# Kernel tuning notes

Measured on AMD Instinct MI355X. Metric: run time of the kernel, lower is better.

## Reference

```python
import jax, jax.numpy as jnp
import numpy as np

B = 128      # puzzles per batch
CELLS = 81
N = B * CELLS
H = 96       # hidden_dim
E_SZ = 16    # embed_size
T = 16       # num_steps


def _sudoku_edges():
    r = np.arange(CELLS) // 9
    c = np.arange(CELLS) % 9
    b = (r // 3) * 3 + (c // 3)
    src, dst = [], []
    for u in range(CELLS):
        for v in range(CELLS):
            if u != v and (r[u] == r[v] or c[u] == c[v] or b[u] == b[v]):
                src.append(u)
                dst.append(v)
    return np.asarray(src, np.int32), np.asarray(dst, np.int32)


def setup_inputs() -> dict:
    key = jax.random.key(0)
    ks = jax.random.split(key, 24)
    s, d = _sudoku_edges()
    off = (np.arange(B, dtype=np.int32) * CELLS)[:, None]
    src = jnp.asarray((s[None, :] + off).reshape(-1))
    dst = jnp.asarray((d[None, :] + off).reshape(-1))
    row = jnp.asarray(np.tile(np.arange(CELLS, dtype=np.int32) // 9, B))
    col = jnp.asarray(np.tile(np.arange(CELLS, dtype=np.int32) % 9, B))
    q = jax.random.randint(ks[0], (N,), 0, 10, dtype=jnp.int32)
    labels = jax.random.randint(ks[1], (N,), 1, 10, dtype=jnp.int32)

    def lin(k, o, i):
        return (jax.random.normal(k, (o, i), jnp.float32) / np.sqrt(i)).astype(jnp.float32)

    d_emb = jax.random.normal(ks[2], (10, E_SZ), jnp.float32)
    r_emb = jax.random.normal(ks[3], (9, E_SZ), jnp.float32)
    c_emb = jax.random.normal(ks[4], (9, E_SZ), jnp.float32)
    in_W0 = lin(ks[5], H, 3 * E_SZ)
    in_W = jnp.stack([lin(ks[6 + i], H, H) for i in range(3)])   # [3,H,H]
    in_b = jnp.zeros((4, H), jnp.float32)
    msg_W0 = lin(ks[9], H, 2 * H)
    msg_W = jnp.stack([lin(ks[10 + i], H, H) for i in range(3)])
    msg_b = jnp.zeros((4, H), jnp.float32)
    # LSTMCell (no bias): input = cat(x, m) of size 2H, hidden H; gate order i,f,g,o
    W_ih = lin(ks[13], 4 * H, 2 * H)
    W_hh = lin(ks[14], 4 * H, H)
    out_W = lin(ks[15], 10, H)
    out_b = jnp.zeros((10,), jnp.float32)
    return dict(q=q, row=row, col=col, labels=labels, src=src, dst=dst,
                d_emb=d_emb, r_emb=r_emb, c_emb=c_emb,
                in_W0=in_W0, in_W=in_W, in_b=in_b,
                msg_W0=msg_W0, msg_W=msg_W, msg_b=msg_b,
                W_ih=W_ih, W_hh=W_hh, out_W=out_W, out_b=out_b)


def _mlp4(x, W0, W, b):
    # Linear,ReLU,Linear,ReLU,Linear,ReLU,Linear
    x = jax.nn.relu(x @ W0.T + b[0])
    x = jax.nn.relu(x @ W[0].T + b[1])
    x = jax.nn.relu(x @ W[1].T + b[2])
    return x @ W[2].T + b[3]


def reference(q, row, col, labels, src, dst, d_emb, r_emb, c_emb,
              in_W0, in_W, in_b, msg_W0, msg_W, msg_b,
              W_ih, W_hh, out_W, out_b):
    x = _mlp4(jnp.concatenate([d_emb[q], r_emb[row], c_emb[col]], -1),
              in_W0, in_W, in_b)                       # [N,H]
    h0 = x
    rh0 = jnp.zeros_like(x)
    rc0 = jnp.zeros_like(x)

    def step(carry, _):
        h, rh, rc = carry
        # per-edge message: MLP(cat(h_src, h_dst)), sum-aggregated into dst
        me = _mlp4(jnp.concatenate([h[src], h[dst]], -1), msg_W0, msg_W, msg_b)
        m = jax.ops.segment_sum(me, dst, num_segments=N)  # [N,H]
        gates = jnp.concatenate([x, m], -1) @ W_ih.T + rh @ W_hh.T
        i, f, g, o = jnp.split(gates, 4, axis=-1)
        nc = jax.nn.sigmoid(f) * rc + jax.nn.sigmoid(i) * jnp.tanh(g)
        nh = jax.nn.sigmoid(o) * jnp.tanh(nc)
        return (nh, nh, nc), nh

    _, hs = jax.lax.scan(step, (h0, rh0, rc0), None, length=T)  # [T,N,H]
    logits = hs @ out_W.T + out_b                               # [T,N,10]
    preds = jnp.argmax(logits, -1)                              # [T,N]
    lf = logits.reshape(-1, 10)
    lab = jnp.tile(labels, T)
    logp = jax.nn.log_softmax(lf, -1)
    loss = -jnp.mean(jnp.take_along_axis(logp, lab[:, None].astype(jnp.int32), 1))
    return preds, loss, lf
```

## Files before the change

### kernel.cpp

```cpp
#include <hip/hip_runtime.h>

#define NN 10368
#define EE 207360
#define TT 16

#define O_W0AT    0
#define O_W0BT    9216
#define O_WHHT    18432
#define O_WIHXT   55296
#define O_WCOMBT  92160
#define O_GB      129024
#define O_LOSS    129408
#define O_WIN0T   129424
#define O_WINT    134032
#define O_H       161680
#define O_C       (O_H  + NN*96)
#define O_A       (O_C  + NN*96)
#define O_BV      (O_A  + NN*96)
#define O_S2      (O_BV + NN*96)
#define O_X       (O_S2 + NN*96)
#define O_WFRAG   (O_X  + NN*96)
#define O_GX      (O_WFRAG + 27648)
#define O_WL2     O_X
#define O_WAB2    (O_X + 110592)
#define SF_WIN0   O_S2
#define SF_WIN    (O_S2 + 9216)
#define SF_WX     (O_S2 + 50688)

using bf16x8 = __attribute__((ext_vector_type(8))) short;
using s16x4  = __attribute__((ext_vector_type(4))) short;
using f32x4  = __attribute__((ext_vector_type(4))) float;

__device__ __forceinline__ float sigm(float x){ return 1.f/(1.f + expf(-x)); }

__device__ __forceinline__ unsigned rne_bf16(float f){
  unsigned u = __float_as_uint(f);
  u += 0x7fffu + ((u >> 16) & 1u);
  return u >> 16;
}
__device__ __forceinline__ void split3(float x, short& h, short& m, short& l){
  unsigned uh = rne_bf16(x); h = (short)uh;
  float fh = __uint_as_float(uh << 16);
  float r1 = x - fh;
  unsigned um = rne_bf16(r1); m = (short)um;
  float fm = __uint_as_float(um << 16);
  float r2 = r1 - fm;
  l = (short)rne_bf16(r2);
}

__device__ __forceinline__ f32x4 mfma6(bf16x8 aH, bf16x8 aM, bf16x8 aL,
                                       bf16x8 WH, bf16x8 WM, bf16x8 WL, f32x4 acc){
  acc = __builtin_amdgcn_mfma_f32_16x16x32_bf16(aH, WH, acc, 0,0,0);
  acc = __builtin_amdgcn_mfma_f32_16x16x32_bf16(aH, WM, acc, 0,0,0);
  acc = __builtin_amdgcn_mfma_f32_16x16x32_bf16(aM, WH, acc, 0,0,0);
  acc = __builtin_amdgcn_mfma_f32_16x16x32_bf16(aH, WL, acc, 0,0,0);
  acc = __builtin_amdgcn_mfma_f32_16x16x32_bf16(aL, WH, acc, 0,0,0);
  acc = __builtin_amdgcn_mfma_f32_16x16x32_bf16(aM, WM, acc, 0,0,0);
  return acc;
}

__device__ __forceinline__ f32x4 mfma6s(bf16x8 WH, bf16x8 WM, bf16x8 WL,
                                        bf16x8 aH, bf16x8 aM, bf16x8 aL, f32x4 acc){
  acc = __builtin_amdgcn_mfma_f32_16x16x32_bf16(WH, aH, acc, 0,0,0);
  acc = __builtin_amdgcn_mfma_f32_16x16x32_bf16(WM, aH, acc, 0,0,0);
  acc = __builtin_amdgcn_mfma_f32_16x16x32_bf16(WH, aM, acc, 0,0,0);
  acc = __builtin_amdgcn_mfma_f32_16x16x32_bf16(WL, aH, acc, 0,0,0);
  acc = __builtin_amdgcn_mfma_f32_16x16x32_bf16(WH, aL, acc, 0,0,0);
  acc = __builtin_amdgcn_mfma_f32_16x16x32_bf16(WM, aM, acc, 0,0,0);
  return acc;
}

__global__ void k_convert(float* ws, const float* msgW0, const float* Whh, const float* Wih,
                          const float* inW0, const float* inW)
{
  int i = blockIdx.x*256 + threadIdx.x;
  if (i < 9216){ int k=i/96, j=i%96; ws[O_W0AT+i] = msgW0[j*192+k];    return; } i -= 9216;
  if (i < 9216){ int k=i/96, j=i%96; ws[O_W0BT+i] = msgW0[j*192+96+k]; return; } i -= 9216;
  if (i < 36864){ int k=i/384, j=i%384; ws[O_WHHT+i]  = Whh[j*96+k];   return; } i -= 36864;
  if (i < 36864){ int k=i/384, j=i%384; ws[O_WIHXT+i] = Wih[j*192+k];  return; } i -= 36864;
  if (i < 4608){ int k=i/96, j=i%96; ws[O_WIN0T+i] = inW0[j*48+k];     return; } i -= 4608;
  if (i < 27648){ int l=i/9216, r=i%9216; int k=r/96, j=r%96;
                  ws[O_WINT+i] = inW[l*9216 + j*96 + k];               return; } i -= 27648;
  if (i == 0){ ws[O_LOSS] = 0.f; }
}

__global__ void k_wfrag(float* ws, const float* msgW)
{
  int idx = blockIdx.x*256 + threadIdx.x;
  if (idx >= 2*3*18*64) return;
  int lane = idx & 63;
  int tile = (idx >> 6) % 18;
  int lev  = (idx >> 6) / 18 % 3;
  int layer= (idx >> 6) / 54;
  int nt = tile/3, kt = tile%3;
  int nout = (lane & 15) + 16*nt;
  int q = lane >> 4;
  unsigned short* wf = (unsigned short*)(ws + O_WFRAG);
  unsigned short* dstp = wf + (size_t)(((layer*3+lev)*18 + tile)*64 + lane)*8;
  const float* W = msgW + layer*9216;
  for (int j=0;j<8;j++){
    float wv = W[nout*96 + 32*kt + 8*q + j];
    short h,m,l; split3(wv, h, m, l);
    dstp[j] = (unsigned short)(lev==0 ? h : (lev==1 ? m : l));
  }
}

__global__ void k_wcomb(float* ws, const float* Wih, const float* msgW, const float* msgb)
{
  int t = blockIdx.x*256 + threadIdx.x;
  if (t >= 36864) return;
  int j = t % 384, qq = t / 384;
  float a0=0.f,a1=0.f,a2=0.f,a3=0.f;
  for (int r=0;r<96;r+=4){
    a0 = fmaf(Wih[j*192+96+r  ], msgW[2*9216+(r  )*96+qq], a0);
    a1 = fmaf(Wih[j*192+96+r+1], msgW[2*9216+(r+1)*96+qq], a1);
    a2 = fmaf(Wih[j*192+96+r+2], msgW[2*9216+(r+2)*96+qq], a2);
    a3 = fmaf(Wih[j*192+96+r+3], msgW[2*9216+(r+3)*96+qq], a3);
  }
  ws[O_WCOMBT + qq*384 + j] = (a0+a1)+(a2+a3);
  if (qq == 0){
    float g=0.f;
    for (int r=0;r<96;r++) g = fmaf(Wih[j*192+96+r], msgb[288+r], g);
    ws[O_GB + j] = 20.f * g;
  }
}

__global__ void k_wl(float* ws)
{
  int idx = blockIdx.x*256 + threadIdx.x;
  if (idx >= 24*6*64) return;
  int L  = idx & 63;
  int ks = (idx >> 6) % 6;
  int nt = (idx >> 6) / 6;
  int col = (L & 15) + 16*nt;
  int q = L >> 4;
  unsigned short* wf = (unsigned short*)(ws + O_WL2);
  for (int j=0;j<8;j++){
    int k = 32*(ks%3) + 8*q + j;
    float wv = (ks < 3) ? ws[O_WCOMBT + k*384 + col] : ws[O_WHHT + k*384 + col];
    short h,m,l; split3(wv, h, m, l);
    wf[(size_t)(((0*24+nt)*6 + ks)*64 + L)*8 + j] = (unsigned short)h;
    wf[(size_t)(((1*24+nt)*6 + ks)*64 + L)*8 + j] = (unsigned short)m;
    wf[(size_t)(((2*24+nt)*6 + ks)*64 + L)*8 + j] = (unsigned short)l;
  }
}

__global__ void k_wab(float* ws)
{
  int idx = blockIdx.x*256 + threadIdx.x;
  if (idx >= 12*3*64) return;
  int L  = idx & 63;
  int ks = (idx >> 6) % 3;
  int nt = (idx >> 6) / 3;
  int col = (L & 15) + 16*nt;
  int q = L >> 4;
  unsigned short* wf = (unsigned short*)(ws + O_WAB2);
  for (int j=0;j<8;j++){
    int k = 32*ks + 8*q + j;
    float wv = (col < 96) ? ws[O_W0AT + k*96 + col] : ws[O_W0BT + k*96 + (col-96)];
    short h,m,l; split3(wv, h, m, l);
    wf[(size_t)(((0*12+nt)*3 + ks)*64 + L)*8 + j] = (unsigned short)h;
    wf[(size_t)(((1*12+nt)*3 + ks)*64 + L)*8 + j] = (unsigned short)m;
    wf[(size_t)(((2*12+nt)*3 + ks)*64 + L)*8 + j] = (unsigned short)l;
  }
}

__global__ void k_wfin(float* ws)
{
  int idx = blockIdx.x*256 + threadIdx.x;
  if (idx >= 138*64) return;
  int L = idx & 63;
  int f = idx >> 6;
  int q = L >> 4, mcol = L & 15;
  if (f < 12){
    int nt = f >> 1, ks = f & 1;
    int col = mcol + 16*nt;
    unsigned short* wp = (unsigned short*)(ws + SF_WIN0);
    for (int j=0;j<8;j++){
      int k = 32*ks + 8*q + j;
      float v = (k < 48) ? ws[O_WIN0T + k*96 + col] : 0.f;
      short h,m,l; split3(v,h,m,l);
      wp[(size_t)((0*12 + f)*64 + L)*8 + j] = (unsigned short)h;
      wp[(size_t)((1*12 + f)*64 + L)*8 + j] = (unsigned short)m;
      wp[(size_t)((2*12 + f)*64 + L)*8 + j] = (unsigned short)l;
    }
  } else if (f < 66){
    int f2 = f - 12;
    int l = f2/18, r2 = f2%18;
    int nt = r2/3, ks = r2%3;
    int col = mcol + 16*nt;
    unsigned short* wp = (unsigned short*)(ws + SF_WIN);
    for (int j=0;j<8;j++){
      int k = 32*ks + 8*q + j;
      float v = ws[O_WINT + l*9216 + k*96 + col];
      short h,m,l2; split3(v,h,m,l2);
      wp[(size_t)((0*54 + f2)*64 + L)*8 + j] = (unsigned short)h;
      wp[(size_t)((1*54 + f2)*64 + L)*8 + j] = (unsigned short)m;
      wp[(size_t)((2*54 + f2)*64 + L)*8 + j] = (unsigned short)l2;
    }
  } else {
    int f3 = f - 66;
    int nt = f3/3, ks = f3%3;
    int col = mcol + 16*nt;
    unsigned short* wp = (unsigned short*)(ws + SF_WX);
    for (int j=0;j<8;j++){
      int k = 32*ks + 8*q + j;
      float v = ws[O_WIHXT + k*384 + col];
      short h,m,l2; split3(v,h,m,l2);
      wp[(size_t)((0*72 + f3)*64 + L)*8 + j] = (unsigned short)h;
      wp[(size_t)((1*72 + f3)*64 + L)*8 + j] = (unsigned short)m;
      wp[(size_t)((2*72 + f3)*64 + L)*8 + j] = (unsigned short)l2;
    }
  }
}

__global__ __launch_bounds__(384) void k_input_mf(float* ws,
    const int* q, const int* row, const int* col,
    const float* demb, const float* remb, const float* cemb,
    const float* inb, const float* msgb)
{
  __shared__ float eintile[16*49];
  __shared__ bf16x8 fA[3][3][64];
  __shared__ bf16x8 fB[3][3][64];
  int tid = threadIdx.x;
  int w = tid >> 6, L = tid & 63;
  int m = L & 15, qd = L >> 4;
  int nb = blockIdx.x*16;
  int colw = 16*w + m;

  for (int idx = tid; idx < 768; idx += 384){
    int ni = idx/48, f = idx%48;
    int n = nb + ni;
    float v;
    if (f < 16)      v = demb[q[n]*16 + f];
    else if (f < 32) v = remb[row[n]*16 + (f-16)];
    else             v = cemb[col[n]*16 + (f-32)];
    eintile[ni*49 + f] = v;
  }
  __syncthreads();

  if (tid < 128){
    int ks = tid >> 6, Ls = tid & 63;
    int node = Ls & 15, qs = Ls >> 4;
    bf16x8 vh, vm, vl;
    #pragma unroll
    for (int j=0;j<8;j++){
      int k = 32*ks + 8*qs + j;
      float v = (k < 48) ? eintile[node*49 + k] : 0.f;
      short hh,mm,ll; split3(v, hh, mm, ll);
      vh[j]=hh; vm[j]=mm; vl[j]=ll;
    }
    fA[0][ks][Ls]=vh; fA[1][ks][Ls]=vm; fA[2][ks][Ls]=vl;
  }
  __syncthreads();

  int kt = colw >> 5, qp = (colw & 31) >> 3, jc = colw & 7;

  f32x4 acc;
  {
    float b0 = inb[colw];
    acc[0]=b0; acc[1]=b0; acc[2]=b0; acc[3]=b0;
    const bf16x8* W = (const bf16x8*)(ws + SF_WIN0);
    #pragma unroll
    for (int ks=0; ks<2; ks++){
      acc = mfma6(fA[0][ks][L], fA[1][ks][L], fA[2][ks][L],
                  W[(size_t)((0*12 + w*2+ks)*64) + L],
                  W[(size_t)((1*12 + w*2+ks)*64) + L],
                  W[(size_t)((2*12 + w*2+ks)*64) + L], acc);
    }
  }
  {
    unsigned short* bp = (unsigned short*)&fB[0][0][0];
    #pragma unroll
    for (int r=0;r<4;r++){
      float v = fmaxf(acc[r], 0.f);
      short hh,mm,ll; split3(v, hh, mm, ll);
      int Lp = 4*qd + r + 16*qp;
      bp[(size_t)((0*3+kt)*64 + Lp)*8 + jc] = (unsigned short)hh;
      bp[(size_t)((1*3+kt)*64 + Lp)*8 + jc] = (unsigned short)mm;
      bp[(size_t)((2*3+kt)*64 + Lp)*8 + jc] = (unsigned short)ll;
    }
  }
  __syncthreads();

  #pragma unroll
  for (int l=0; l<3; l++){
    bf16x8 (*src)[3][64] = (l & 1) ? fA : fB;
    bf16x8 (*dstb)[3][64] = (l & 1) ? fB : fA;
    float bl = inb[(l+1)*96 + colw];
    acc[0]=bl; acc[1]=bl; acc[2]=bl; acc[3]=bl;
    const bf16x8* W = (const bf16x8*)(ws + SF_WIN);
    #pragma unroll
    for (int ks=0; ks<3; ks++){
      acc = mfma6(src[0][ks][L], src[1][ks][L], src[2][ks][L],
                  W[(size_t)((0*54 + l*18 + w*3+ks)*64) + L],
                  W[(size_t)((1*54 + l*18 + w*3+ks)*64) + L],
                  W[(size_t)((2*54 + l*18 + w*3+ks)*64) + L], acc);
    }
    if (l < 2){
      unsigned short* bp = (unsigned short*)&dstb[0][0][0];
      #pragma unroll
      for (int r=0;r<4;r++){
        float v = fmaxf(acc[r], 0.f);
        short hh,mm,ll; split3(v, hh, mm, ll);
        int Lp = 4*qd + r + 16*qp;
        bp[(size_t)((0*3+kt)*64 + Lp)*8 + jc] = (unsigned short)hh;
        bp[(size_t)((1*3+kt)*64 + Lp)*8 + jc] = (unsigned short)mm;
        bp[(size_t)((2*3+kt)*64 + Lp)*8 + jc] = (unsigned short)ll;
      }
      __syncthreads();
    }
  }
  {
    unsigned short* bp = (unsigned short*)&fA[0][0][0];
    #pragma unroll
    for (int r=0;r<4;r++){
      int n = nb + 4*qd + r;
      ws[O_H + (size_t)n*96 + colw] = acc[r];
      ws[O_C + (size_t)n*96 + colw] = 0.f;
      short hh,mm,ll; split3(acc[r], hh, mm, ll);
      int Lp = 4*qd + r + 16*qp;
      bp[(size_t)((0*3+kt)*64 + Lp)*8 + jc] = (unsigned short)hh;
      bp[(size_t)((1*3+kt)*64 + Lp)*8 + jc] = (unsigned short)mm;
      bp[(size_t)((2*3+kt)*64 + Lp)*8 + jc] = (unsigned short)ll;
    }
  }
  __syncthreads();

  {
    const bf16x8* wab = (const bf16x8*)(ws + O_WAB2);
    f32x4 accA = {0.f,0.f,0.f,0.f};
    f32x4 accB = {0.f,0.f,0.f,0.f};
    #pragma unroll
    for (int ks=0; ks<3; ks++){
      bf16x8 hH = fA[0][ks][L], hM = fA[1][ks][L], hL = fA[2][ks][L];
      accA = mfma6(hH, hM, hL,
                   wab[(size_t)(((0*12+w)*3 + ks)*64) + L],
                   wab[(size_t)(((1*12+w)*3 + ks)*64) + L],
                   wab[(size_t)(((2*12+w)*3 + ks)*64) + L], accA);
      accB = mfma6(hH, hM, hL,
                   wab[(size_t)(((0*12+w+6)*3 + ks)*64) + L],
                   wab[(size_t)(((1*12+w+6)*3 + ks)*64) + L],
                   wab[(size_t)(((2*12+w+6)*3 + ks)*64) + L], accB);
    }
    float b0v = msgb[colw];
    #pragma unroll
    for (int r=0; r<4; r++){
      int n = nb + 4*qd + r;
      ws[O_A  + (size_t)n*96 + colw] = accA[r];
      ws[O_BV + (size_t)n*96 + colw] = accB[r] + b0v;
    }
  }

  {
    const bf16x8* wx = (const bf16x8*)(ws + SF_WX);
    #pragma unroll
    for (int g=0; g<4; g++){
      int nt = w + 6*g;
      int c384 = m + 16*nt;
      float gbv = ws[O_GB + c384];
      f32x4 ag; ag[0]=gbv; ag[1]=gbv; ag[2]=gbv; ag[3]=gbv;
      #pragma unroll
      for (int ks=0; ks<3; ks++){
        ag = mfma6(fA[0][ks][L], fA[1][ks][L], fA[2][ks][L],
                   wx[(size_t)((0*72 + nt*3+ks)*64) + L],
                   wx[(size_t)((1*72 + nt*3+ks)*64) + L],
                   wx[(size_t)((2*72 + nt*3+ks)*64) + L], ag);
      }
      *(f32x4*)(ws + O_GX + (size_t)c384*NN + nb + 4*qd) = ag;
    }
  }
}

__global__ __launch_bounds__(192) void k_input(float* ws,
    const int* q, const int* row, const int* col,
    const float* demb, const float* remb, const float* cemb,
    const float* inb, const float* msgb)
{
  __shared__ float ein[2][8*49];
  __shared__ float hb[2][8*97];
  int tid = threadIdx.x; int g = tid/96, j = tid%96;
  int nq = blockIdx.x*2 + g; int n0 = nq*8;

  for (int idx=j; idx<384; idx+=96){
    int i = idx/48, f = idx%48; int n = n0+i;
    float v;
    if (f < 16)      v = demb[q[n]*16 + f];
    else if (f < 32) v = remb[row[n]*16 + (f-16)];
    else             v = cemb[col[n]*16 + (f-32)];
    ein[g][i*49+f] = v;
  }
  __syncthreads();

  float acc[8];
  {
    const float* W0T = ws + O_WIN0T;
    float b0 = inb[j];
    #pragma unroll
    for (int i=0;i<8;i++) acc[i]=b0;
    #pragma unroll 2
    for (int k=0;k<48;k++){
      float w = W0T[k*96+j];
      #pragma unroll
      for (int i=0;i<8;i++) acc[i] = fmaf(w, ein[g][i*49+k], acc[i]);
    }
    #pragma unroll
    for (int i=0;i<8;i++) hb[g][i*97+j] = fmaxf(acc[i], 0.f);
  }
  __syncthreads();

  for (int l=0;l<3;l++){
    const float* WT = ws + O_WINT + l*9216;
    float bl = inb[(l+1)*96 + j];
    #pragma unroll
    for (int i=0;i<8;i++) acc[i]=bl;
    #pragma unroll 2
    for (int k=0;k<96;k++){
      float w = WT[k*96+j];
      #pragma unroll
      for (int i=0;i<8;i++) acc[i] = fmaf(w, hb[g][i*97+k], acc[i]);
    }
    __syncthreads();
    if (l < 2){
      #pragma unroll
      for (int i=0;i<8;i++) hb[g][i*97+j] = fmaxf(acc[i], 0.f);
    } else {
      #pragma unroll
      for (int i=0;i<8;i++) hb[g][i*97+j] = acc[i];
    }
    __syncthreads();
  }

  float* h = ws + O_H; float* c = ws + O_C; float* x = ws + O_X;
  #pragma unroll
  for (int i=0;i<8;i++){
    int n = n0+i;
    float vv = hb[g][i*97+j];
    h[n*96+j]=vv; x[n*96+j]=vv; c[n*96+j]=0.f;
  }
  const float* WA = ws + O_W0AT; const float* WB = ws + O_W0BT;
  float aa[8], ab[8];
  #pragma unroll
  for (int i=0;i<8;i++){ aa[i]=0.f; ab[i]=0.f; }
  #pragma unroll 2
  for (int k=0;k<96;k++){
    float wa=WA[k*96+j], wb=WB[k*96+j];
    #pragma unroll
    for (int i=0;i<8;i++){
      float hv = hb[g][i*97+k];
      aa[i]=fmaf(wa,hv,aa[i]); ab[i]=fmaf(wb,hv,ab[i]);
    }
  }
  float* A=ws+O_A; float* Bv=ws+O_BV;
  float b0v = msgb[j];
  #pragma unroll
  for (int i=0;i<8;i++){ int n=n0+i; A[n*96+j]=aa[i]; Bv[n*96+j]=ab[i]+b0v; }
}

__global__ __launch_bounds__(384) void k_edge(float* ws, const int* dst, const float* msgb)
{
  __shared__ bf16x8 aF[45][64];
  int tid = threadIdx.x;
  int w = tid >> 6, L = tid & 63;
  int q = L >> 4, m = L & 15;
  int n0 = blockIdx.x*4;
  int e0 = blockIdx.x*80;
  const unsigned short* wf = (const unsigned short*)(ws + O_WFRAG);
  const float* Aact = ws + O_A;
  const float* Bact = ws + O_BV;

  for (int idx = tid; idx < 960; idx += 384){
    int mt = idx / 192;
    int kt = (idx % 192) / 64;
    int Ls = idx & 63;
    int el = mt*16 + (Ls & 15);
    int v  = dst[e0 + el];
    int n  = n0 + el/20;
    int k0 = 32*kt + 8*(Ls >> 4);
    float4 a0 = *(const float4*)(Aact + (size_t)v*96 + k0);
    float4 a1 = *(const float4*)(Aact + (size_t)v*96 + k0 + 4);
    float4 b0 = *(const float4*)(Bact + (size_t)n*96 + k0);
    float4 b1 = *(const float4*)(Bact + (size_t)n*96 + k0 + 4);
    float r[8];
    r[0]=fmaxf(a0.x+b0.x,0.f); r[1]=fmaxf(a0.y+b0.y,0.f);
    r[2]=fmaxf(a0.z+b0.z,0.f); r[3]=fmaxf(a0.w+b0.w,0.f);
    r[4]=fmaxf(a1.x+b1.x,0.f); r[5]=fmaxf(a1.y+b1.y,0.f);
    r[6]=fmaxf(a1.z+b1.z,0.f); r[7]=fmaxf(a1.w+b1.w,0.f);
    bf16x8 vh, vm, vl;
    #pragma unroll
    for (int j=0;j<8;j++){
      short hh,mm,ll; split3(r[j], hh, mm, ll);
      vh[j]=hh; vm[j]=mm; vl[j]=ll;
    }
    aF[0*15 + mt*3 + kt][Ls] = vh;
    aF[1*15 + mt*3 + kt][Ls] = vm;
    aF[2*15 + mt*3 + kt][Ls] = vl;
  }
  __syncthreads();

  f32x4 rD[5];
  {
    bf16x8 W1[3][3];
    #pragma unroll
    for (int lev=0; lev<3; lev++)
      #pragma unroll
      for (int kt2=0; kt2<3; kt2++)
        W1[lev][kt2] = ((const bf16x8*)wf)[(size_t)((0*3+lev)*18 + w*3+kt2)*64 + L];
    float4 bb4 = *(const float4*)(msgb + 96 + 16*w + 4*q);
    #pragma unroll
    for (int nt=0; nt<5; nt++){
      f32x4 acc = {0.f,0.f,0.f,0.f};
      #pragma unroll
      for (int kt2=0; kt2<3; kt2++){
        acc = mfma6s(W1[0][kt2], W1[1][kt2], W1[2][kt2],
                     aF[0*15+nt*3+kt2][L], aF[1*15+nt*3+kt2][L], aF[2*15+nt*3+kt2][L],
                     acc);
      }
      rD[nt][0] = fmaxf(acc[0] + bb4.x, 0.f);
      rD[nt][1] = fmaxf(acc[1] + bb4.y, 0.f);
      rD[nt][2] = fmaxf(acc[2] + bb4.z, 0.f);
      rD[nt][3] = fmaxf(acc[3] + bb4.w, 0.f);
    }
  }
  __syncthreads();

  {
    int ktw = w >> 1;
    int qs  = 2*(w & 1) + (q >> 1);
    int Lp  = m + 16*qs;
    int j0  = (q & 1)*4;
    unsigned short* af16 = (unsigned short*)&aF[0][0];
    #pragma unroll
    for (int nt=0; nt<5; nt++){
      s16x4 vh4, vm4, vl4;
      #pragma unroll
      for (int r=0; r<4; r++){
        short hh,mm,ll; split3(rD[nt][r], hh, mm, ll);
        vh4[r]=hh; vm4[r]=mm; vl4[r]=ll;
      }
      *(s16x4*)(af16 + (size_t)((0*15+nt*3+ktw)*64 + Lp)*8 + j0) = vh4;
      *(s16x4*)(af16 + (size_t)((1*15+nt*3+ktw)*64 + Lp)*8 + j0) = vm4;
      *(s16x4*)(af16 + (size_t)((2*15+nt*3+ktw)*64 + Lp)*8 + j0) = vl4;
    }
  }
  __syncthreads();

  {
    bf16x8 W2[3][3];
    #pragma unroll
    for (int lev=0; lev<3; lev++)
      #pragma unroll
      for (int kt2=0; kt2<3; kt2++)
        W2[lev][kt2] = ((const bf16x8*)wf)[(size_t)((1*3+lev)*18 + w*3+kt2)*64 + L];
    float bb = msgb[192 + 16*w + m];
    float sn[4] = {0.f,0.f,0.f,0.f};
    #pragma unroll
    for (int mt=0; mt<5; mt++){
      f32x4 acc = {0.f,0.f,0.f,0.f};
      #pragma unroll
      for (int kt2=0; kt2<3; kt2++){
        acc = mfma6(aF[0*15+mt*3+kt2][L], aF[1*15+mt*3+kt2][L], aF[2*15+mt*3+kt2][L],
                    W2[0][kt2], W2[1][kt2], W2[2][kt2], acc);
      }
      #pragma unroll
      for (int r=0;r<4;r++){
        int el = mt*16 + 4*q + r;
        float o = fmaxf(acc[r] + bb, 0.f);
        sn[el/20] += o;
      }
    }
    #pragma unroll
    for (int nd=0; nd<4; nd++){
      sn[nd] += __shfl_xor(sn[nd], 16);
      sn[nd] += __shfl_xor(sn[nd], 32);
    }
    if (L < 16){
      float* s2 = ws + O_S2;
      #pragma unroll
      for (int nd=0; nd<4; nd++)
        s2[(size_t)(n0+nd)*96 + 16*w + m] = sn[nd];
    }
  }
}

__global__ __launch_bounds__(384) void k_lstm_mf(float* ws, const int* labels,
                                                 const float* msgb,
                                                 const float* outW, const float* outb,
                                                 float* out, int t)
{
  __shared__ bf16x8 aF[3][384];
  __shared__ bf16x8 hF[3][192];
  __shared__ float sh2[16*100];
  __shared__ float lgt[160];
  int tid = threadIdx.x;
  int w = tid >> 6, L = tid & 63;
  int m = L & 15, q = L >> 4;
  int nb = blockIdx.x*16;
  const float hscale = (t == 0) ? 0.f : 1.f;

  {
    int ks = tid/64; int Ls = tid%64;
    int node = nb + (Ls & 15); int qs = Ls >> 4;
    const float* src = (ks < 3) ? (ws + O_S2 + (size_t)node*96 + 32*ks + 8*qs)
                                : (ws + O_H  + (size_t)node*96 + 32*(ks-3) + 8*qs);
    float sc = (ks < 3) ? 1.f : hscale;
    float4 v0 = *(const float4*)src;
    float4 v1 = *(const float4*)(src + 4);
    float r[8] = {v0.x,v0.y,v0.z,v0.w,v1.x,v1.y,v1.z,v1.w};
    bf16x8 vh, vm, vl;
    #pragma unroll
    for (int j=0;j<8;j++){
      short hh,mm,ll; split3(r[j]*sc, hh, mm, ll);
      vh[j]=hh; vm[j]=mm; vl[j]=ll;
    }
    aF[0][tid]=vh; aF[1][tid]=vm; aF[2][tid]=vl;
  }

  f32x4 acc[4];
  #pragma unroll
  for (int g=0; g<4; g++){
    int c384 = m + 16*(w + 6*g);
    acc[g] = *(const f32x4*)(ws + O_GX + (size_t)c384*NN + nb + 4*q);
  }
  __syncthreads();

  const bf16x8* wl = (const bf16x8*)(ws + O_WL2);
  #pragma unroll 2
  for (int ks=0; ks<6; ks++){
    bf16x8 aH = aF[0][ks*64+L], aM = aF[1][ks*64+L], aLw = aF[2][ks*64+L];
    #pragma unroll
    for (int g=0; g<4; g++){
      int nt = w + 6*g;
      bf16x8 WH = wl[(size_t)(((0*24+nt)*6 + ks)*64) + L];
      bf16x8 WM = wl[(size_t)(((1*24+nt)*6 + ks)*64) + L];
      bf16x8 WL = wl[(size_t)(((2*24+nt)*6 + ks)*64) + L];
      acc[g] = mfma6(aH, aM, aLw, WH, WM, WL, acc[g]);
    }
  }

  {
    int jj = m + 16*w;
    #pragma unroll
    for (int r=0; r<4; r++){
      int n = nb + q*4 + r;
      float ig = sigm(acc[0][r]);
      float fg = sigm(acc[1][r]);
      float gg = tanhf(acc[2][r]);
      float og = sigm(acc[3][r]);
      float cv = ws[O_C + (size_t)n*96 + jj];
      float nc = fg*cv + ig*gg;
      float nv = og*tanhf(nc);
      ws[O_C + (size_t)n*96 + jj] = nc;
      ws[O_H + (size_t)n*96 + jj] = nv;
      sh2[(q*4 + r)*100 + jj] = nv;
    }
  }
  __syncthreads();

  if (tid < 192){
    int ks = tid/64; int Ls = tid%64; int qs = Ls >> 4;
    const float* src = &sh2[(Ls & 15)*100 + 32*ks + 8*qs];
    float4 v0 = *(const float4*)src;
    float4 v1 = *(const float4*)(src + 4);
    float r[8] = {v0.x,v0.y,v0.z,v0.w,v1.x,v1.y,v1.z,v1.w};
    bf16x8 vh, vm, vl;
    #pragma unroll
    for (int j=0;j<8;j++){
      short hh,mm,ll; split3(r[j], hh, mm, ll);
      vh[j]=hh; vm[j]=mm; vl[j]=ll;
    }
    hF[0][tid]=vh; hF[1][tid]=vm; hF[2][tid]=vl;
  }
  __syncthreads();

  {
    const bf16x8* wab = (const bf16x8*)(ws + O_WAB2);
    f32x4 accA = {0.f,0.f,0.f,0.f};
    f32x4 accB = {0.f,0.f,0.f,0.f};
    #pragma unroll
    for (int ks=0; ks<3; ks++){
      bf16x8 hH = hF[0][ks*64+L], hM = hF[1][ks*64+L], hLw = hF[2][ks*64+L];
      accA = mfma6(hH, hM, hLw,
                   wab[(size_t)(((0*12+w)*3 + ks)*64) + L],
                   wab[(size_t)(((1*12+w)*3 + ks)*64) + L],
                   wab[(size_t)(((2*12+w)*3 + ks)*64) + L], accA);
      accB = mfma6(hH, hM, hLw,
                   wab[(size_t)(((0*12+w+6)*3 + ks)*64) + L],
                   wab[(size_t)(((1*12+w+6)*3 + ks)*64) + L],
                   wab[(size_t)(((2*12+w+6)*3 + ks)*64) + L], accB);
    }
    int jj = m + 16*w;
    float b0v = msgb[jj];
    #pragma unroll
    for (int r=0; r<4; r++){
      int n = nb + q*4 + r;
      ws[O_A  + (size_t)n*96 + jj] = accA[r];
      ws[O_BV + (size_t)n*96 + jj] = accB[r] + b0v;
    }
  }

  if (tid < 160){
    int ln = tid/10, cls = tid%10;
    int n = nb + ln;
    float q0=outb[cls], q1=0.f, q2=0.f, q3v=0.f;
    const float* hr = &sh2[ln*100];
    #pragma unroll
    for (int k=0;k<96;k+=4){
      q0=fmaf(outW[cls*96+k  ],hr[k  ],q0);  q1=fmaf(outW[cls*96+k+1],hr[k+1],q1);
      q2=fmaf(outW[cls*96+k+2],hr[k+2],q2);  q3v=fmaf(outW[cls*96+k+3],hr[k+3],q3v);
    }
    float lgv = (q0+q1)+(q2+q3v);
    lgt[ln*10 + cls] = lgv;
    out[165889 + ((size_t)t*NN + n)*10 + cls] = lgv;
  }
  __syncthreads();
  if (tid < 16){
    int n = nb + tid;
    const float* Lg = &lgt[tid*10];
    float mx = Lg[0]; int bi = 0;
    #pragma unroll
    for (int cc=1;cc<10;cc++){ if (Lg[cc] > mx){ mx=Lg[cc]; bi=cc; } }
    float se = 0.f;
    #pragma unroll
    for (int cc=0;cc<10;cc++) se += expf(Lg[cc]-mx);
    int lab = labels[n];
    float lp = Lg[lab] - mx - logf(se);
    atomicAdd(ws + O_LOSS, -lp);
    out[t*NN + n] = (float)bi;
  }
}

__global__ __launch_bounds__(384) void k_lstm_valu(float* ws, const int* labels,
                                                   const float* msgb,
                                                   const float* outW, const float* outb,
                                                   float* out, int t)
{
  __shared__ float ss[768], sh[768], sx[768];
  __shared__ float lg[8*384];
  __shared__ float lh[8*97];
  __shared__ float lgt[80];
  int tid = threadIdx.x;
  int nb = blockIdx.x*8;
  const float* WC = ws + O_WCOMBT;
  const float* WH = ws + O_WHHT;
  float* h = ws + O_H; float* c = ws + O_C;
  const float hscale = (t == 0) ? 0.f : 1.f;

  for (int idx = tid; idx < 768; idx += 384){
    ss[idx] = ws[O_S2 + (size_t)nb*96 + idx];
    sh[idx] = ws[O_H  + (size_t)nb*96 + idx] * hscale;
    sx[idx] = ws[O_X + (size_t)nb*96 + idx];
  }
  float acc[8];
  float gb = ws[O_GB + tid];
  #pragma unroll
  for (int i=0;i<8;i++) acc[i] = gb;
  __syncthreads();

  {
    const float* WX = ws + O_WIHXT;
    #pragma unroll 2
    for (int k0=0;k0<96;k0+=4){
      float4 xv[8];
      #pragma unroll
      for (int i=0;i<8;i++) xv[i] = *(const float4*)&sx[i*96+k0];
      #pragma unroll
      for (int kk=0;kk<4;kk++){
        float w = WX[(k0+kk)*384 + tid];
        #pragma unroll
        for (int i=0;i<8;i++){
          float xe = (kk==0)?xv[i].x:(kk==1)?xv[i].y:(kk==2)?xv[i].z:xv[i].w;
          acc[i] = fmaf(w, xe, acc[i]);
        }
      }
    }
  }

  #pragma unroll 2
  for (int k0=0;k0<96;k0+=4){
    float4 sv[8], rv[8];
    #pragma unroll
    for (int i=0;i<8;i++){
      sv[i] = *(const float4*)&ss[i*96+k0];
      rv[i] = *(const float4*)&sh[i*96+k0];
    }
    #pragma unroll
    for (int kk=0;kk<4;kk++){
      float cw = WC[(k0+kk)*384 + tid];
      float hw = WH[(k0+kk)*384 + tid];
      #pragma unroll
      for (int i=0;i<8;i++){
        float se = (kk==0)?sv[i].x:(kk==1)?sv[i].y:(kk==2)?sv[i].z:sv[i].w;
        float re = (kk==0)?rv[i].x:(kk==1)?rv[i].y:(kk==2)?rv[i].z:rv[i].w;
        acc[i] = fmaf(cw, se, fmaf(hw, re, acc[i]));
      }
    }
  }
  #pragma unroll
  for (int i=0;i<8;i++) lg[i*384 + tid] = acc[i];
  __syncthreads();

  #pragma unroll
  for (int half=0; half<2; half++){
    int p = tid + half*384;
    int i = p/96, jj = p%96;
    int n = nb + i;
    float ig = sigm(lg[i*384 + jj]);
    float fg = sigm(lg[i*384 + 96 + jj]);
    float gg = tanhf(lg[i*384 + 192 + jj]);
    float og = sigm(lg[i*384 + 288 + jj]);
    float cv = c[(size_t)n*96 + jj];
    float nc = fg*cv + ig*gg;
    float nv = og*tanhf(nc);
    c[(size_t)n*96 + jj] = nc;
    h[(size_t)n*96 + jj] = nv;
    lh[i*97 + jj] = nv;
  }
  __syncthreads();

  {
    const float* WA = ws + O_W0AT; const float* WB = ws + O_W0BT;
    int q3 = tid/96, jj = tid%96;
    int i0 = q3*2;
    float aa0=0.f, aa1=0.f, ab0=0.f, ab1=0.f;
    #pragma unroll 2
    for (int k=0;k<96;k++){
      float wa = WA[k*96+jj], wb = WB[k*96+jj];
      float h0v = lh[i0*97 + k], h1v = lh[(i0+1)*97 + k];
      aa0 = fmaf(wa, h0v, aa0); ab0 = fmaf(wb, h0v, ab0);
      aa1 = fmaf(wa, h1v, aa1); ab1 = fmaf(wb, h1v, ab1);
    }
    float b0v = msgb[jj];
    float* Aa = ws + O_A; float* Bb = ws + O_BV;
    Aa[(size_t)(nb+i0)*96 + jj]   = aa0; Bb[(size_t)(nb+i0)*96 + jj]   = ab0 + b0v;
    Aa[(size_t)(nb+i0+1)*96 + jj] = aa1; Bb[(size_t)(nb+i0+1)*96 + jj] = ab1 + b0v;
  }

  if (tid < 80){
    int ln = tid/10, cls = tid%10;
    int n = nb + ln;
    float q0=outb[cls], q1=0.f, q2=0.f, q3v=0.f;
    const float* hr = &lh[ln*97];
    #pragma unroll
    for (int k=0;k<96;k+=4){
      q0=fmaf(outW[cls*96+k  ],hr[k  ],q0);  q1=fmaf(outW[cls*96+k+1],hr[k+1],q1);
      q2=fmaf(outW[cls*96+k+2],hr[k+2],q2);  q3v=fmaf(outW[cls*96+k+3],hr[k+3],q3v);
    }
    float lgv = (q0+q1)+(q2+q3v);
    lgt[ln*10 + cls] = lgv;
    out[165889 + ((size_t)t*NN + n)*10 + cls] = lgv;
  }
  __syncthreads();
  if (tid < 8){
    int n = nb + tid;
    const float* Lg = &lgt[tid*10];
    float mx = Lg[0]; int bi = 0;
    #pragma unroll
    for (int cc=1;cc<10;cc++){ if (Lg[cc] > mx){ mx=Lg[cc]; bi=cc; } }
    float se = 0.f;
    #pragma unroll
    for (int cc=0;cc<10;cc++) se += expf(Lg[cc]-mx);
    int lab = labels[n];
    float lp = Lg[lab] - mx - logf(se);
    atomicAdd(ws + O_LOSS, -lp);
    out[t*NN + n] = (float)bi;
  }
}

__global__ void k_final(float* ws, float* out){
  if (threadIdx.x == 0 && blockIdx.x == 0)
    out[165888] = ws[O_LOSS] / (float)(TT*NN);
}

extern "C" void kernel_launch(void* const* d_in, const int* in_sizes, int n_in,
                              void* d_out, int out_size, void* d_ws, size_t ws_size,
                              hipStream_t stream)
{
  (void)in_sizes; (void)n_in; (void)out_size;
  const int* q      = (const int*)d_in[0];
  const int* row    = (const int*)d_in[1];
  const int* col    = (const int*)d_in[2];
  const int* labels = (const int*)d_in[3];
  const int* dst    = (const int*)d_in[5];
  const float* demb  = (const float*)d_in[6];
  const float* remb  = (const float*)d_in[7];
  const float* cemb  = (const float*)d_in[8];
  const float* inW0  = (const float*)d_in[9];
  const float* inW   = (const float*)d_in[10];
  const float* inb   = (const float*)d_in[11];
  const float* msgW0 = (const float*)d_in[12];
  const float* msgW  = (const float*)d_in[13];
  const float* msgb  = (const float*)d_in[14];
  const float* Wih   = (const float*)d_in[15];
  const float* Whh   = (const float*)d_in[16];
  const float* outW  = (const float*)d_in[17];
  const float* outb  = (const float*)d_in[18];

  float* ws  = (float*)d_ws;
  float* out = (float*)d_out;

  const size_t need_gx = ((size_t)O_GX + (size_t)NN*384) * sizeof(float);
  const int use_mf = (ws_size >= need_gx) ? 1 : 0;

  hipLaunchKernelGGL(k_convert, dim3(487), dim3(256), 0, stream,
                     ws, msgW0, Whh, Wih, inW0, inW);
  hipLaunchKernelGGL(k_wfrag, dim3(27), dim3(256), 0, stream, ws, msgW);
  hipLaunchKernelGGL(k_wcomb, dim3(144), dim3(256), 0, stream, ws, Wih, msgW, msgb);
  if (use_mf){
    hipLaunchKernelGGL(k_wfin, dim3(35), dim3(256), 0, stream, ws);
    hipLaunchKernelGGL(k_wl,  dim3(36), dim3(256), 0, stream, ws);
    hipLaunchKernelGGL(k_wab, dim3(9),  dim3(256), 0, stream, ws);
    hipLaunchKernelGGL(k_input_mf, dim3(648), dim3(384), 0, stream,
                       ws, q, row, col, demb, remb, cemb, inb, msgb);
  } else {
    hipLaunchKernelGGL(k_input, dim3(648), dim3(192), 0, stream,
                       ws, q, row, col, demb, remb, cemb, inb, msgb);
  }
  for (int t=0; t<TT; ++t){
    hipLaunchKernelGGL(k_edge, dim3(EE/80), dim3(384), 0, stream, ws, dst, msgb);
    if (use_mf)
      hipLaunchKernelGGL(k_lstm_mf, dim3(NN/16), dim3(384), 0, stream,
                         ws, labels, msgb, outW, outb, out, t);
    else
      hipLaunchKernelGGL(k_lstm_valu, dim3(1296), dim3(384), 0, stream,
                         ws, labels, msgb, outW, outb, out, t);
  }
  hipLaunchKernelGGL(k_final, dim3(1), dim3(64), 0, stream, ws, out);
}
```

Before: 1.616 ms.

## Use MFMA for output logits, remap block order, prefetch LSTM state early

The output projection to 10 logits moves from scalar FMA loops in 160 threads to a 3-way split bf16 MFMA on one wavefront, with outW pre-split into fragments in k_wfin. Block indices in the input, edge and LSTM kernels are permuted so consecutive blocks cover different puzzles, which may change L2 and XCD locality. The cell state and gate preloads are issued before the shared-memory conversion so their latency overlaps it. The h fragment conversion now uses all 384 threads with half-width vectors. Together these aim to cut per-step LSTM kernel time, at the cost of a small precision difference in the logits and some extra setup work.

Result: no change. 1.610 ms (-0.4%).

```diff
diff --git a/kernel.cpp b/kernel.cpp
--- a/kernel.cpp
+++ b/kernel.cpp
@@ -23,6 +23,7 @@
 #define O_GX      (O_WFRAG + 27648)
 #define O_WL2     O_X
 #define O_WAB2    (O_X + 110592)
+#define O_WO      (O_X + 138240)
 #define SF_WIN0   O_S2
 #define SF_WIN    (O_S2 + 9216)
 #define SF_WX     (O_S2 + 50688)
@@ -165,10 +166,10 @@
   }
 }
 
-__global__ void k_wfin(float* ws)
+__global__ void k_wfin(float* ws, const float* outW)
 {
   int idx = blockIdx.x*256 + threadIdx.x;
-  if (idx >= 138*64) return;
+  if (idx >= 141*64) return;
   int L = idx & 63;
   int f = idx >> 6;
   int q = L >> 4, mcol = L & 15;
@@ -198,7 +199,7 @@
       wp[(size_t)((1*54 + f2)*64 + L)*8 + j] = (unsigned short)m;
       wp[(size_t)((2*54 + f2)*64 + L)*8 + j] = (unsigned short)l2;
     }
-  } else {
+  } else if (f < 138){
     int f3 = f - 66;
     int nt = f3/3, ks = f3%3;
     int col = mcol + 16*nt;
@@ -211,6 +212,17 @@
       wp[(size_t)((1*72 + f3)*64 + L)*8 + j] = (unsigned short)m;
       wp[(size_t)((2*72 + f3)*64 + L)*8 + j] = (unsigned short)l2;
     }
+  } else {
+    int ks = f - 138;
+    unsigned short* wp = (unsigned short*)(ws + O_WO);
+    for (int j=0;j<8;j++){
+      int k = 32*ks + 8*q + j;
+      float v = (mcol < 10) ? outW[mcol*96 + k] : 0.f;
+      short h,m,l2; split3(v,h,m,l2);
+      wp[(size_t)((0*3 + ks)*64 + L)*8 + j] = (unsigned short)h;
+      wp[(size_t)((1*3 + ks)*64 + L)*8 + j] = (unsigned short)m;
+      wp[(size_t)((2*3 + ks)*64 + L)*8 + j] = (unsigned short)l2;
+    }
   }
 }
 
@@ -225,7 +237,8 @@
   int tid = threadIdx.x;
   int w = tid >> 6, L = tid & 63;
   int m = L & 15, qd = L >> 4;
-  int nb = blockIdx.x*16;
+  int b2 = blockIdx.x; b2 = (b2 & 7)*81 + (b2 >> 3);
+  int nb = b2*16;
   int colw = 16*w + m;
 
   for (int idx = tid; idx < 768; idx += 384){
@@ -463,8 +476,11 @@
   int tid = threadIdx.x;
   int w = tid >> 6, L = tid & 63;
   int q = L >> 4, m = L & 15;
-  int n0 = blockIdx.x*4;
-  int e0 = blockIdx.x*80;
+  int g4 = blockIdx.x >> 2;
+  g4 = (g4 & 7)*81 + (g4 >> 3);
+  int bid = g4*4 + (blockIdx.x & 3);
+  int n0 = bid*4;
+  int e0 = bid*80;
   const unsigned short* wf = (const unsigned short*)(ws + O_WFRAG);
   const float* Aact = ws + O_A;
   const float* Bact = ws + O_BV;
@@ -591,12 +607,27 @@
   __shared__ bf16x8 aF[3][384];
   __shared__ bf16x8 hF[3][192];
   __shared__ float sh2[16*100];
-  __shared__ float lgt[160];
+  __shared__ float lgt[256];
   int tid = threadIdx.x;
   int w = tid >> 6, L = tid & 63;
   int m = L & 15, q = L >> 4;
-  int nb = blockIdx.x*16;
+  int b2 = blockIdx.x; b2 = (b2 & 7)*81 + (b2 >> 3);
+  int nb = b2*16;
   const float hscale = (t == 0) ? 0.f : 1.f;
+
+  float cpre[4];
+  {
+    int jj = m + 16*w;
+    #pragma unroll
+    for (int r=0; r<4; r++)
+      cpre[r] = ws[O_C + (size_t)(nb + q*4 + r)*96 + jj];
+  }
+  f32x4 acc[4];
+  #pragma unroll
+  for (int g=0; g<4; g++){
+    int c384 = m + 16*(w + 6*g);
+    acc[g] = *(const f32x4*)(ws + O_GX + (size_t)c384*NN + nb + 4*q);
+  }
 
   {
     int ks = tid/64; int Ls = tid%64;
@@ -615,13 +646,6 @@
     }
     aF[0][tid]=vh; aF[1][tid]=vm; aF[2][tid]=vl;
   }
-
-  f32x4 acc[4];
-  #pragma unroll
-  for (int g=0; g<4; g++){
-    int c384 = m + 16*(w + 6*g);
-    acc[g] = *(const f32x4*)(ws + O_GX + (size_t)c384*NN + nb + 4*q);
-  }
   __syncthreads();
 
   const bf16x8* wl = (const bf16x8*)(ws + O_WL2);
@@ -647,8 +671,7 @@
       float fg = sigm(acc[1][r]);
       float gg = tanhf(acc[2][r]);
       float og = sigm(acc[3][r]);
-      float cv = ws[O_C + (size_t)n*96 + jj];
-      float nc = fg*cv + ig*gg;
+      float nc = fg*cpre[r] + ig*gg;
       float nv = og*tanhf(nc);
       ws[O_C + (size_t)n*96 + jj] = nc;
       ws[O_H + (size_t)n*96 + jj] = nv;
@@ -657,19 +680,25 @@
   }
   __syncthreads();
 
-  if (tid < 192){
-    int ks = tid/64; int Ls = tid%64; int qs = Ls >> 4;
-    const float* src = &sh2[(Ls & 15)*100 + 32*ks + 8*qs];
+  {
+    int s = tid >> 1;
+    int ks = s/64, Ls = s%64, qs = Ls >> 4;
+    int half = tid & 1;
+    const float* src = &sh2[(Ls & 15)*100 + 32*ks + 8*qs + 4*half];
     float4 v0 = *(const float4*)src;
-    float4 v1 = *(const float4*)(src + 4);
-    float r[8] = {v0.x,v0.y,v0.z,v0.w,v1.x,v1.y,v1.z,v1.w};
-    bf16x8 vh, vm, vl;
-    #pragma unroll
-    for (int j=0;j<8;j++){
-      short hh,mm,ll; split3(r[j], hh, mm, ll);
+    s16x4 vh, vm, vl;
+    float rr[4] = {v0.x, v0.y, v0.z, v0.w};
+    #pragma unroll
+    for (int j=0;j<4;j++){
+      short hh,mm,ll; split3(rr[j], hh, mm, ll);
       vh[j]=hh; vm[j]=mm; vl[j]=ll;
     }
-    hF[0][tid]=vh; hF[1][tid]=vm; hF[2][tid]=vl;
+    unsigned short* hp0 = (unsigned short*)&hF[0][s];
+    unsigned short* hp1 = (unsigned short*)&hF[1][s];
+    unsigned short* hp2 = (unsigned short*)&hF[2][s];
+    *(s16x4*)(hp0 + 4*half) = vh;
+    *(s16x4*)(hp1 + 4*half) = vm;
+    *(s16x4*)(hp2 + 4*half) = vl;
   }
   __syncthreads();
 
@@ -699,24 +728,29 @@
     }
   }
 
-  if (tid < 160){
-    int ln = tid/10, cls = tid%10;
-    int n = nb + ln;
-    float q0=outb[cls], q1=0.f, q2=0.f, q3v=0.f;
-    const float* hr = &sh2[ln*100];
-    #pragma unroll
-    for (int k=0;k<96;k+=4){
-      q0=fmaf(outW[cls*96+k  ],hr[k  ],q0);  q1=fmaf(outW[cls*96+k+1],hr[k+1],q1);
-      q2=fmaf(outW[cls*96+k+2],hr[k+2],q2);  q3v=fmaf(outW[cls*96+k+3],hr[k+3],q3v);
-    }
-    float lgv = (q0+q1)+(q2+q3v);
-    lgt[ln*10 + cls] = lgv;
-    out[165889 + ((size_t)t*NN + n)*10 + cls] = lgv;
+  if (w == 0){
+    const bf16x8* wo = (const bf16x8*)(ws + O_WO);
+    float ob = (m < 10) ? outb[m] : 0.f;
+    f32x4 lacc; lacc[0]=ob; lacc[1]=ob; lacc[2]=ob; lacc[3]=ob;
+    #pragma unroll
+    for (int ks=0; ks<3; ks++){
+      lacc = mfma6(hF[0][ks*64+L], hF[1][ks*64+L], hF[2][ks*64+L],
+                   wo[(size_t)((0*3 + ks)*64) + L],
+                   wo[(size_t)((1*3 + ks)*64) + L],
+                   wo[(size_t)((2*3 + ks)*64) + L], lacc);
+    }
+    #pragma unroll
+    for (int r=0; r<4; r++){
+      int n = nb + 4*q + r;
+      lgt[(4*q + r)*16 + m] = lacc[r];
+      if (m < 10)
+        out[165889 + ((size_t)t*NN + n)*10 + m] = lacc[r];
+    }
   }
   __syncthreads();
   if (tid < 16){
     int n = nb + tid;
-    const float* Lg = &lgt[tid*10];
+    const float* Lg = &lgt[tid*16];
     float mx = Lg[0]; int bi = 0;
     #pragma unroll
     for (int cc=1;cc<10;cc++){ if (Lg[cc] > mx){ mx=Lg[cc]; bi=cc; } }
@@ -907,7 +941,7 @@
   hipLaunchKernelGGL(k_wfrag, dim3(27), dim3(256), 0, stream, ws, msgW);
   hipLaunchKernelGGL(k_wcomb, dim3(144), dim3(256), 0, stream, ws, Wih, msgW, msgb);
   if (use_mf){
-    hipLaunchKernelGGL(k_wfin, dim3(35), dim3(256), 0, stream, ws);
+    hipLaunchKernelGGL(k_wfin, dim3(36), dim3(256), 0, stream, ws, outW);
     hipLaunchKernelGGL(k_wl,  dim3(36), dim3(256), 0, stream, ws);
     hipLaunchKernelGGL(k_wab, dim3(9),  dim3(256), 0, stream, ws);
     hipLaunchKernelGGL(k_input_mf, dim3(648), dim3(384), 0, stream,
```
